# Optimization experiments

Measured on AMD Instinct MI355X. Metric: run time of the kernel, lower is better.

The kernel has to match this reference:

```python
import jax, jax.numpy as jnp
import numpy as np

Z, I, J, K = 131072, 32, 32, 64  # points, in-channels 1, in-channels 2, out-channels
DENSITY = 0.08  # Clebsch-Gordan mixing matrices are highly sparse


def setup_inputs() -> dict:
    key = jax.random.key(0)
    k1, k2, k3, k4 = jax.random.split(key, 4)
    features_1 = jax.random.normal(k1, (Z, I), dtype=jnp.float32)
    features_2 = jax.random.normal(k2, (Z, J), dtype=jnp.float32)
    # matching the structural sparsity of rs.elementwise_tensor_product output.
    vals = jax.random.normal(k3, (K, I, J), dtype=jnp.float32)
    mask = jax.random.uniform(k4, (K, I, J)) < DENSITY
    mixing_matrix = jnp.where(mask, vals, 0.0).astype(jnp.float32)
    return {"features_1": features_1, "features_2": features_2, "mixing_matrix": mixing_matrix}


def reference(features_1, features_2, mixing_matrix):
    # Faithful to torch: output[z,k] = sum_{i,j} mixing[k,i,j] * f1[z,i] * f2[z,j]
    # (leading dims are already flat: features are [Z, channels])
    return jnp.einsum('kij,zi,zj->zk', mixing_matrix, features_1, features_2)
```

## Files before the change

### kernel.cpp

```cpp
#include <hip/hip_runtime.h>

typedef _Float16 h2 __attribute__((ext_vector_type(2)));
typedef _Float16 h8 __attribute__((ext_vector_type(8)));
typedef float f32x4 __attribute__((ext_vector_type(4)));

#define ZPTS 131072
#define GRPBYTES 16384

__global__ void etp_prep(const float* __restrict__ mix, _Float16* __restrict__ w) {
  int t = blockIdx.x * 256 + threadIdx.x;
  int n = t >> 10;
  int c = t & 1023;
  float v = mix[t];
  int g = c >> 7;
  int off = (n << 8) + ((c & 127) << 1);
  off ^= (n & 7) << 4;
  *reinterpret_cast<_Float16*>(reinterpret_cast<char*>(w) + g * GRPBYTES + off) =
      (_Float16)v;
}

__global__ __launch_bounds__(256, 2) void etp_main(
    const float* __restrict__ f1, const float* __restrict__ f2,
    const _Float16* __restrict__ w, float* __restrict__ out) {
  __shared__ char lds[2 * GRPBYTES];
  const int tid = threadIdx.x;
  const int lane = tid & 63;
  const int wv = tid >> 6;
  const int l15 = lane & 15;
  const int lhi = lane >> 4;
  const int j0 = lhi << 3;
  const int zw = blockIdx.x * 256 + wv * 64;

  h2 f2h[4][4];
  int zr[4];
#pragma unroll
  for (int m = 0; m < 4; ++m) {
    int z = zw + m * 16 + l15;
    zr[m] = z;
    const float4* p = reinterpret_cast<const float4*>(f2 + z * 32 + j0);
    float4 a = p[0];
    float4 b = p[1];
    f2h[m][0] = h2{(_Float16)a.x, (_Float16)a.y};
    f2h[m][1] = h2{(_Float16)a.z, (_Float16)a.w};
    f2h[m][2] = h2{(_Float16)b.x, (_Float16)b.y};
    f2h[m][3] = h2{(_Float16)b.z, (_Float16)b.w};
  }

  f32x4 acc[4][4];
#pragma unroll
  for (int m = 0; m < 4; ++m)
#pragma unroll
    for (int n = 0; n < 4; ++n) acc[m][n] = f32x4{0.f, 0.f, 0.f, 0.f};

  auto stage = [&](int g, int buf) {
#pragma unroll
    for (int q = 0; q < 4; ++q) {
      int idx = (wv << 2) + q;
      const char* gp = reinterpret_cast<const char*>(w) + g * GRPBYTES +
                       idx * 1024 + lane * 16;
      __builtin_amdgcn_global_load_lds(
          (const __attribute__((address_space(1))) void*)gp,
          (__attribute__((address_space(3))) void*)(lds + buf * GRPBYTES + idx * 1024),
          16, 0, 0);
    }
  };

  stage(0, 0);

#pragma unroll 1
  for (int g = 0; g < 8; ++g) {
    float4 f1v[4];
#pragma unroll
    for (int m = 0; m < 4; ++m)
      f1v[m] = *reinterpret_cast<const float4*>(f1 + zr[m] * 32 + g * 4);

    __syncthreads();
    if (g < 7) stage(g + 1, (g + 1) & 1);
    const char* B = lds + (g & 1) * GRPBYTES;

#pragma unroll
    for (int cc = 0; cc < 4; ++cc) {
      h8 bf[4];
#pragma unroll
      for (int nt = 0; nt < 4; ++nt) {
        int rw = nt * 16 + l15;
        int off = ((rw << 8) + ((cc * 32 + j0) << 1)) ^ ((rw & 7) << 4);
        bf[nt] = *reinterpret_cast<const h8*>(B + off);
      }
#pragma unroll
      for (int m = 0; m < 4; ++m) {
        float f1s = (cc == 0) ? f1v[m].x
                  : (cc == 1) ? f1v[m].y
                  : (cc == 2) ? f1v[m].z : f1v[m].w;
        _Float16 fh = (_Float16)f1s;
        h2 f1h = h2{fh, fh};
        union { h8 v; h2 h[4]; } af;
        af.h[0] = f1h * f2h[m][0];
        af.h[1] = f1h * f2h[m][1];
        af.h[2] = f1h * f2h[m][2];
        af.h[3] = f1h * f2h[m][3];
#pragma unroll
        for (int nt = 0; nt < 4; ++nt)
          acc[m][nt] =
              __builtin_amdgcn_mfma_f32_16x16x32_f16(af.v, bf[nt], acc[m][nt], 0, 0, 0);
      }
    }
  }

#pragma unroll
  for (int m = 0; m < 4; ++m) {
    int zbase = zw + m * 16 + lhi * 4;
#pragma unroll
    for (int r = 0; r < 4; ++r) {
      float* o = out + (zbase + r) * 64 + l15;
      o[0] = acc[m][0][r];
      o[16] = acc[m][1][r];
      o[32] = acc[m][2][r];
      o[48] = acc[m][3][r];
    }
  }
}

extern "C" void kernel_launch(void* const* d_in, const int* in_sizes, int n_in,
                              void* d_out, int out_size, void* d_ws, size_t ws_size,
                              hipStream_t stream) {
  const float* f1 = (const float*)d_in[0];
  const float* f2 = (const float*)d_in[1];
  const float* mix = (const float*)d_in[2];
  float* out = (float*)d_out;
  _Float16* w = (_Float16*)d_ws;

  hipLaunchKernelGGL(etp_prep, dim3(256), dim3(256), 0, stream, mix, w);
  hipLaunchKernelGGL(etp_main, dim3(ZPTS / 256), dim3(256), 0, stream, f1, f2, w, out);
}
```

Measured before the change: 98.95 us.

## Halve rows per block, raise occupancy, prefetch f1 and vectorize prep

Each wave now handles 32 points instead of 64, so the grid doubles and launch bounds request 4 blocks per SM to raise occupancy and latency hiding. The f1 slice for the next group is loaded one iteration ahead so its global latency overlaps the current group's MFMAs. The prep kernel converts 8 weights per thread with vector loads and stores. The trade-off is that each block stages the full weight matrix into LDS for half as many points, which doubles weight traffic per output.

```diff
diff --git a/kernel.cpp b/kernel.cpp
--- a/kernel.cpp
+++ b/kernel.cpp
@@ -5,78 +5,85 @@
 typedef float f32x4 __attribute__((ext_vector_type(4)));
 
 #define ZPTS 131072
-#define GRPBYTES 16384
+#define GRPB 16384
 
 __global__ void etp_prep(const float* __restrict__ mix, _Float16* __restrict__ w) {
   int t = blockIdx.x * 256 + threadIdx.x;
-  int n = t >> 10;
-  int c = t & 1023;
-  float v = mix[t];
+  int base = t * 8;
+  int n = base >> 10;
+  int c = base & 1023;
+  const float4* src = reinterpret_cast<const float4*>(mix + base);
+  float4 a = src[0], b = src[1];
+  h8 v;
+  v[0] = (_Float16)a.x; v[1] = (_Float16)a.y; v[2] = (_Float16)a.z; v[3] = (_Float16)a.w;
+  v[4] = (_Float16)b.x; v[5] = (_Float16)b.y; v[6] = (_Float16)b.z; v[7] = (_Float16)b.w;
   int g = c >> 7;
-  int off = (n << 8) + ((c & 127) << 1);
-  off ^= (n & 7) << 4;
-  *reinterpret_cast<_Float16*>(reinterpret_cast<char*>(w) + g * GRPBYTES + off) =
-      (_Float16)v;
+  int off = ((n << 8) + ((c & 127) << 1)) ^ ((n & 7) << 4);
+  *reinterpret_cast<h8*>(reinterpret_cast<char*>(w) + g * GRPB + off) = v;
 }
 
-__global__ __launch_bounds__(256, 2) void etp_main(
+__global__ __launch_bounds__(256, 4) void etp_main(
     const float* __restrict__ f1, const float* __restrict__ f2,
     const _Float16* __restrict__ w, float* __restrict__ out) {
-  __shared__ char lds[2 * GRPBYTES];
+  __shared__ __align__(16) char lds[2 * GRPB];
   const int tid = threadIdx.x;
   const int lane = tid & 63;
   const int wv = tid >> 6;
   const int l15 = lane & 15;
   const int lhi = lane >> 4;
   const int j0 = lhi << 3;
-  const int zw = blockIdx.x * 256 + wv * 64;
+  const int zw = blockIdx.x * 128 + wv * 32;
 
-  h2 f2h[4][4];
-  int zr[4];
+  h2 f2h[2][4];
+  int zr[2];
 #pragma unroll
-  for (int m = 0; m < 4; ++m) {
+  for (int m = 0; m < 2; ++m) {
     int z = zw + m * 16 + l15;
     zr[m] = z;
     const float4* p = reinterpret_cast<const float4*>(f2 + z * 32 + j0);
-    float4 a = p[0];
-    float4 b = p[1];
+    float4 a = p[0], b = p[1];
     f2h[m][0] = h2{(_Float16)a.x, (_Float16)a.y};
     f2h[m][1] = h2{(_Float16)a.z, (_Float16)a.w};
     f2h[m][2] = h2{(_Float16)b.x, (_Float16)b.y};
     f2h[m][3] = h2{(_Float16)b.z, (_Float16)b.w};
   }
 
-  f32x4 acc[4][4];
+  f32x4 acc[2][4];
 #pragma unroll
-  for (int m = 0; m < 4; ++m)
+  for (int m = 0; m < 2; ++m)
 #pragma unroll
     for (int n = 0; n < 4; ++n) acc[m][n] = f32x4{0.f, 0.f, 0.f, 0.f};
 
-  auto stage = [&](int g, int buf) {
+  auto stageW = [&](int g, int p) {
 #pragma unroll
     for (int q = 0; q < 4; ++q) {
       int idx = (wv << 2) + q;
-      const char* gp = reinterpret_cast<const char*>(w) + g * GRPBYTES +
-                       idx * 1024 + lane * 16;
+      const char* gp =
+          reinterpret_cast<const char*>(w) + g * GRPB + idx * 1024 + lane * 16;
       __builtin_amdgcn_global_load_lds(
           (const __attribute__((address_space(1))) void*)gp,
-          (__attribute__((address_space(3))) void*)(lds + buf * GRPBYTES + idx * 1024),
+          (__attribute__((address_space(3))) void*)(lds + p * GRPB + idx * 1024),
           16, 0, 0);
     }
   };
 
-  stage(0, 0);
+  stageW(0, 0);
+  float4 f1cur[2];
+#pragma unroll
+  for (int m = 0; m < 2; ++m)
+    f1cur[m] = *reinterpret_cast<const float4*>(f1 + zr[m] * 32);
 
 #pragma unroll 1
   for (int g = 0; g < 8; ++g) {
-    float4 f1v[4];
+    __syncthreads();
+    float4 f1nxt[2];
+    if (g < 7) {
+      stageW(g + 1, (g + 1) & 1);
 #pragma unroll
-    for (int m = 0; m < 4; ++m)
-      f1v[m] = *reinterpret_cast<const float4*>(f1 + zr[m] * 32 + g * 4);
-
-    __syncthreads();
-    if (g < 7) stage(g + 1, (g + 1) & 1);
-    const char* B = lds + (g & 1) * GRPBYTES;
+      for (int m = 0; m < 2; ++m)
+        f1nxt[m] = *reinterpret_cast<const float4*>(f1 + zr[m] * 32 + (g + 1) * 4);
+    }
+    const char* B = lds + (g & 1) * GRPB;
 
 #pragma unroll
     for (int cc = 0; cc < 4; ++cc) {
@@ -88,10 +95,10 @@
         bf[nt] = *reinterpret_cast<const h8*>(B + off);
       }
 #pragma unroll
-      for (int m = 0; m < 4; ++m) {
-        float f1s = (cc == 0) ? f1v[m].x
-                  : (cc == 1) ? f1v[m].y
-                  : (cc == 2) ? f1v[m].z : f1v[m].w;
+      for (int m = 0; m < 2; ++m) {
+        float f1s = (cc == 0) ? f1cur[m].x
+                  : (cc == 1) ? f1cur[m].y
+                  : (cc == 2) ? f1cur[m].z : f1cur[m].w;
         _Float16 fh = (_Float16)f1s;
         h2 f1h = h2{fh, fh};
         union { h8 v; h2 h[4]; } af;
@@ -105,10 +112,14 @@
               __builtin_amdgcn_mfma_f32_16x16x32_f16(af.v, bf[nt], acc[m][nt], 0, 0, 0);
       }
     }
+    if (g < 7) {
+#pragma unroll
+      for (int m = 0; m < 2; ++m) f1cur[m] = f1nxt[m];
+    }
   }
 
 #pragma unroll
-  for (int m = 0; m < 4; ++m) {
+  for (int m = 0; m < 2; ++m) {
     int zbase = zw + m * 16 + lhi * 4;
 #pragma unroll
     for (int r = 0; r < 4; ++r) {
@@ -130,6 +141,6 @@
   float* out = (float*)d_out;
   _Float16* w = (_Float16*)d_ws;
 
-  hipLaunchKernelGGL(etp_prep, dim3(256), dim3(256), 0, stream, mix, w);
-  hipLaunchKernelGGL(etp_main, dim3(ZPTS / 256), dim3(256), 0, stream, f1, f2, w, out);
+  hipLaunchKernelGGL(etp_prep, dim3(32), dim3(256), 0, stream, mix, w);
+  hipLaunchKernelGGL(etp_main, dim3(ZPTS / 128), dim3(256), 0, stream, f1, f2, w, out);
 }
```

After: 98.19 us, median of 2. No clear change (-0.8%).
